# Optimization experiments

Measured on AMD Instinct MI355X. Metric: run time of the kernel, lower is better.

## Reference

```python
import jax, jax.numpy as jnp
import numpy as np

B, S, T = 1024, 1024, 32  # batch, seq_len, num_tags


def setup_inputs() -> dict:
    key = jax.random.key(0)
    k1, k2, k3, k4 = jax.random.split(key, 4)
    logits = jax.random.normal(k1, (B, S, T), dtype=jnp.float32)
    transitions = jax.random.normal(k2, (T, T), dtype=jnp.float32)
    tags = jax.random.randint(k3, (B, S), 0, T)
    lengths = jax.random.randint(k4, (B,), 1, S + 1)
    return {"logits": logits, "transitions": transitions, "tags": tags, "lengths": lengths}


def _forward_alg(logits, transitions):
    # viterbi_0 = logits[:, 0, :]; then for t>=1:
    # v_next[b, j] = logsumexp_i(v[b, i] + trans[i, j]) + logits[b, t, j]
    v0 = logits[:, 0, :]  # (B, T)
    emits = jnp.swapaxes(logits[:, 1:, :], 0, 1)  # (S-1, B, T)

    def step(v, emit_t):
        v_next = jax.nn.logsumexp(v[:, :, None] + transitions[None, :, :], axis=1) + emit_t
        return v_next, None

    v_final, _ = jax.lax.scan(step, v0, emits)
    return jax.nn.logsumexp(v_final, axis=1)  # (B,)


def _score_sentence(logits, transitions, tags, lengths):
    # emission scores of gold tags, masked to t < length (note: original ignores
    # lengths in the forward algorithm but uses them here, faithfully reproduced)
    emit = jnp.take_along_axis(logits, tags[:, :, None], axis=2)[..., 0]  # (B, S)
    pos = jnp.arange(S)
    emit_mask = (pos[None, :] < lengths[:, None]).astype(logits.dtype)
    score = jnp.sum(emit * emit_mask, axis=1)
    # transition scores trans[tags[t-1], tags[t]] for 1 <= t < length
    trans_sc = transitions[tags[:, :-1], tags[:, 1:]]  # (B, S-1)
    trans_mask = (pos[None, 1:] < lengths[:, None]).astype(logits.dtype)
    score = score + jnp.sum(trans_sc * trans_mask, axis=1)
    return score  # (B,)


def reference(logits, transitions, tags, lengths):
    log_z = _forward_alg(logits, transitions)
    gold = _score_sentence(logits, transitions, tags, lengths)
    return jnp.mean(log_z - gold)
```

## Files before the change

kernel.cpp:

```cpp
#include <hip/hip_runtime.h>

#define NB 1024
#define NS 1024
#define NT 32
#define L2E 1.44269504088896340736f
#define LN2 0.69314718055994530942f

typedef short        bfrag  __attribute__((ext_vector_type(8)));
typedef float        cfrag  __attribute__((ext_vector_type(16)));
typedef __bf16       bf16x2 __attribute__((ext_vector_type(2)));
typedef float        f32x8  __attribute__((ext_vector_type(8)));
typedef float        f32x4  __attribute__((ext_vector_type(4)));
typedef float        f32x2  __attribute__((ext_vector_type(2)));
typedef unsigned int u32;
typedef unsigned int u32x2v __attribute__((ext_vector_type(2)));
typedef unsigned int u32x4  __attribute__((ext_vector_type(4)));

__device__ __forceinline__ float fexp2(float x){ return __builtin_amdgcn_exp2f(x); }
__device__ __forceinline__ float flog2(float x){ return __builtin_amdgcn_logf(x); }

__device__ __forceinline__ u32 pkbf_rne(float a, float b){
    f32x2 t; t.x = a; t.y = b;
    return __builtin_bit_cast(u32, __builtin_convertvector(t, bf16x2));
}
__device__ __forceinline__ u32 pkbf_t(float a, float b){
    return __builtin_amdgcn_perm(__builtin_bit_cast(u32, b),
                                 __builtin_bit_cast(u32, a), 0x07060302u);
}
__device__ __forceinline__ bfrag mk_afrag(f32x8 v){
    u32x4 r;
    r[0] = pkbf_rne(v[0], v[1]); r[1] = pkbf_rne(v[2], v[3]);
    r[2] = pkbf_rne(v[4], v[5]); r[3] = pkbf_rne(v[6], v[7]);
    return __builtin_bit_cast(bfrag, r);
}

#if __has_builtin(__builtin_amdgcn_permlane32_swap)
#define HAVE_PLSWAP 1
#else
#define HAVE_PLSWAP 0
#endif

__device__ __forceinline__ void half_swap(u32 &x, u32 &y, int h){
#if HAVE_PLSWAP
    u32x2v r = __builtin_amdgcn_permlane32_swap(x, y, false, false);
    x = r[0]; y = r[1];
#else
    u32 X  = __shfl_xor(h ? x : y, 32, 64);
    u32 nx = h ? X : x;
    u32 ny = h ? y : X;
    x = nx; y = ny;
#endif
}

template<int N> struct ic { static constexpr int value = N; };
union accu { cfrag c; f32x2 p[8]; };
union q4u  { f32x4 v; f32x2 p[2]; };

__global__ __launch_bounds__(256, 8) void crf_chunk(
    const float* __restrict__ logits, const float* __restrict__ trans,
    u32* __restrict__ wmat, float* __restrict__ woff)
{
    __shared__ __align__(16) float dscall[4 * 512];

    const int tid = threadIdx.x;
    const int wv  = tid >> 6, lt = tid & 63;
    const int m   = lt & 31,  h  = lt >> 5;
    const int bc  = blockIdx.x * 4 + wv;
    const int b   = bc >> 3,  c  = bc & 7;
    float* dsc = dscall + wv * 512;

    const float* base = logits + (size_t)b * NS * NT;

    f32x8 Et0, Et1;
    #pragma unroll
    for (int j = 0; j < 8; j++){
        Et0[j] = fexp2(L2E * trans[(     8*h + j)*NT + m]);
        Et1[j] = fexp2(L2E * trans[(16 + 8*h + j)*NT + m]);
    }
    const bfrag A0f = mk_afrag(Et0);
    const bfrag A1f = mk_afrag(Et1);

    u32x4 B0v, B1v;
    #pragma unroll
    for (int d = 0; d < 4; d++){
        int k0 = 8*h + 2*d;      u32 v = 0;
        if (k0     == m) v |= 0x3F80u;
        if (k0 + 1 == m) v |= 0x3F800000u;
        B0v[d] = v;
        int k1 = 16 + 8*h + 2*d; v = 0;
        if (k1     == m) v |= 0x3F80u;
        if (k1 + 1 == m) v |= 0x3F800000u;
        B1v[d] = v;
    }

    cfrag zacc;
    #pragma unroll
    for (int q = 0; q < 16; q++) zacc[q] = 0.0f;

    int   offi = 0;
    float exf  = 0.0f;
    const int tbeg = c*128 + 1;

    float eA[4], eB[4];

    auto issue = [&](float (&e)[4], int k){
        const int t0 = tbeg + k*8 + 4*h;
        #pragma unroll
        for (int i = 0; i < 4; i++){
            int t = t0 + i; t = t > (NS-1) ? (NS-1) : t;
            e[i] = base[t*NT + m];
        }
    };
    auto commit = [&](float (&e)[4], int k){
        float* sp = dsc + (k & 1)*256 + (4*h)*32 + m;
        float a0 = (h == 0) ? -exf : 0.0f;
        sp[0]    = fexp2(fmaf(L2E, e[0], a0));
        sp[32]   = fexp2(L2E * e[1]);
        sp[64]   = fexp2(L2E * e[2]);
        sp[96]   = fexp2(L2E * e[3]);
    };

    auto exref = [&](float ref)->int{
        u32 xb = __builtin_bit_cast(u32, ref);
        u32 xf = __builtin_amdgcn_readfirstlane(xb);
        int ex = (int)((xf >> 23) & 0xFFu) - 127;
        return ex < -120 ? -120 : (ex > 120 ? 120 : ex);
    };

    auto procN = [&](int k, bool defer, auto nstc){
        constexpr int NST = decltype(nstc)::value;
        const float* db = dsc + (k & 1)*256 + 4*h;
        #pragma unroll
        for (int i = 0; i < NST; i++){
            accu acc;
            acc.c = __builtin_amdgcn_mfma_f32_32x32x16_bf16(
                        A0f, __builtin_bit_cast(bfrag, B0v), zacc, 0, 0, 0);
            acc.c = __builtin_amdgcn_mfma_f32_32x32x16_bf16(
                        A1f, __builtin_bit_cast(bfrag, B1v), acc.c, 0, 0, 0);

            q4u d0, d1, d2, d3;
            d0.v = *(const f32x4*)(db + i*32 +  0);
            d1.v = *(const f32x4*)(db + i*32 +  8);
            d2.v = *(const f32x4*)(db + i*32 + 16);
            d3.v = *(const f32x4*)(db + i*32 + 24);
            acc.p[0] *= d0.p[0]; acc.p[1] *= d0.p[1];
            acc.p[2] *= d1.p[0]; acc.p[3] *= d1.p[1];
            acc.p[4] *= d2.p[0]; acc.p[5] *= d2.p[1];
            acc.p[6] *= d3.p[0]; acc.p[7] *= d3.p[1];

            if (i == 3){
                int ex = exref(fmaxf(acc.c[0], acc.c[8]));
                offi += ex;
                f32x2 s2;
                s2.x = s2.y = __builtin_bit_cast(float, (u32)(127 - ex) << 23);
                #pragma unroll
                for (int q = 0; q < 8; q++) acc.p[q] *= s2;
            }
            if (i == 7 && defer){
                int ex = exref(fmaxf(acc.c[0], acc.c[8]));
                offi += ex;
                exf = (float)ex;
            }

            u32 P0 = pkbf_t(acc.c[0],  acc.c[1]),  P1 = pkbf_t(acc.c[2],  acc.c[3]);
            u32 P2 = pkbf_t(acc.c[4],  acc.c[5]),  P3 = pkbf_t(acc.c[6],  acc.c[7]);
            u32 P4 = pkbf_t(acc.c[8],  acc.c[9]),  P5 = pkbf_t(acc.c[10], acc.c[11]);
            u32 P6 = pkbf_t(acc.c[12], acc.c[13]), P7 = pkbf_t(acc.c[14], acc.c[15]);
            half_swap(P0, P2, h); half_swap(P1, P3, h);
            half_swap(P4, P6, h); half_swap(P5, P7, h);
            B0v[0]=P0; B0v[1]=P1; B0v[2]=P2; B0v[3]=P3;
            B1v[0]=P4; B1v[1]=P5; B1v[2]=P6; B1v[3]=P7;
        }
    };

    issue(eA, 0); commit(eA, 0);
    #pragma unroll 1
    for (int k = 0; k < 14; k += 2){
        issue(eB, k + 1);
        procN(k, true, ic<8>{});
        commit(eB, k + 1);
        issue(eA, k + 2);
        procN(k + 1, true, ic<8>{});
        commit(eA, k + 2);
    }
    issue(eB, 15);
    procN(14, true, ic<8>{});
    commit(eB, 15);
    if (c != 7) procN(15, false, ic<8>{});
    else        procN(15, false, ic<7>{});

    const size_t mb = (size_t)bc * 512;
    #pragma unroll
    for (int d = 0; d < 4; d++){
        wmat[mb + d*64 + lt]     = B0v[d];
        wmat[mb + (4+d)*64 + lt] = B1v[d];
    }
    if (lt == 0) woff[bc] = (float)offi;
}

__global__ __launch_bounds__(64) void crf_combine(
    const float* __restrict__ logits, const float* __restrict__ trans,
    const int* __restrict__ tags, const int* __restrict__ lens,
    const u32* __restrict__ wmat, const float* __restrict__ woff,
    float* __restrict__ out)
{
    __shared__ __align__(16) float ldsT[NT*NT];
    __shared__ __align__(16) int   ldsTag[NS];
    __shared__ __align__(16) float ldsU[NT];

    const int tid = threadIdx.x;
    const int m   = tid & 31;
    const int b   = blockIdx.x;
    const int len = lens[b];
    const float* lgb = logits + (size_t)b * NS * NT;

    #pragma unroll
    for (int i = 0; i < 16; i++) ldsT[tid + i*64] = trans[tid + i*64];
    const int4* tg4 = (const int4*)(tags + b*NS);
    #pragma unroll
    for (int i = 0; i < 4; i++) ((int4*)ldsTag)[tid + i*64] = tg4[tid + i*64];
    __syncthreads();

    float g = 0.0f;
    #pragma unroll
    for (int it = 0; it < 16; it++){
        int t = tid + it*64;
        if (t < len){
            int tg = ldsTag[t];
            g += lgb[t*NT + tg];
            if (t >= 1) g += ldsT[ldsTag[t-1]*NT + tg];
        }
    }

    float v = fexp2(L2E * lgb[m]);
    float voff = 0.0f;

    const int n  = m;
    const int f  = n >> 4;
    const int hh = (n >> 3) & 1;
    const int di = f*4 + ((n >> 1) & 3);

    for (int cc = 0; cc < 8; cc++){
        const int bcn = b*8 + cc;
        float offc = woff[bcn];
        float w = flog2(v) + offc;
        float mw = w;
        #pragma unroll
        for (int d = 1; d <= 16; d <<= 1) mw = fmaxf(mw, __shfl_xor(mw, d, 64));
        float u = fexp2(w - mw);
        if (tid < 32) ldsU[m] = u;
        __syncthreads();

        const uint4* mp = (const uint4*)(wmat + (size_t)bcn*512 + di*64 + hh*32);
        float acc = 0.0f;
        #pragma unroll
        for (int qq = 0; qq < 8; qq++){
            uint4  md = mp[qq];
            float4 uu = ((const float4*)ldsU)[qq];
            float e0 = __builtin_bit_cast(float, (n&1) ? (md.x & 0xFFFF0000u) : (md.x << 16));
            float e1 = __builtin_bit_cast(float, (n&1) ? (md.y & 0xFFFF0000u) : (md.y << 16));
            float e2 = __builtin_bit_cast(float, (n&1) ? (md.z & 0xFFFF0000u) : (md.z << 16));
            float e3 = __builtin_bit_cast(float, (n&1) ? (md.w & 0xFFFF0000u) : (md.w << 16));
            acc = fmaf(e0, uu.x, acc);
            acc = fmaf(e1, uu.y, acc);
            acc = fmaf(e2, uu.z, acc);
            acc = fmaf(e3, uu.w, acc);
        }
        v = acc;
        voff += mw;
        __syncthreads();
    }

    float s = v;
    #pragma unroll
    for (int d = 1; d <= 16; d <<= 1) s += __shfl_xor(s, d, 64);
    #pragma unroll
    for (int d = 1; d <= 32; d <<= 1) g += __shfl_xor(g, d, 64);
    if (tid == 0){
        float logz = LN2 * (voff + flog2(s));
        atomicAdd(out, (logz - g) * (1.0f / (float)NB));
    }
}

extern "C" void kernel_launch(void* const* d_in, const int* in_sizes, int n_in,
                              void* d_out, int out_size, void* d_ws, size_t ws_size,
                              hipStream_t stream) {
    const float* logits = (const float*)d_in[0];
    const float* trans  = (const float*)d_in[1];
    const int*   tags   = (const int*)d_in[2];
    const int*   lens   = (const int*)d_in[3];

    u32*   wmat = (u32*)d_ws;
    float* woff = (float*)(wmat + 8192*512);

    hipMemsetAsync(d_out, 0, sizeof(float), stream);
    crf_chunk  <<<2048, 256, 0, stream>>>(logits, trans, wmat, woff);
    crf_combine<<<1024, 64, 0, stream>>>(logits, trans, tags, lens, wmat, woff,
                                         (float*)d_out);
}
```

Before: 263.7 us.

## Fold emission scaling into MFMA A-operand and drop LDS staging

Instead of multiplying the MFMA output by per-row emission factors staged through shared memory, each step rebuilds the A fragment as exp(trans) scaled by exp(emission) and packs it to bf16. The per-block rescale multiply on the accumulator is also folded into the next step's emission factor. This removes the LDS writes and reads and the post-MFMA multiplies, and loads each thread's emissions directly into registers with triple buffering. In exchange it adds eight packed multiplies and bf16 packs per step, uses more registers (launch bounds lowered from 8 to 4 blocks per CU), and truncates the scaled matrix to bf16 rather than rounding it.

```diff
diff --git a/kernel.cpp b/kernel.cpp
--- a/kernel.cpp
+++ b/kernel.cpp
@@ -9,8 +9,6 @@
 typedef short        bfrag  __attribute__((ext_vector_type(8)));
 typedef float        cfrag  __attribute__((ext_vector_type(16)));
 typedef __bf16       bf16x2 __attribute__((ext_vector_type(2)));
-typedef float        f32x8  __attribute__((ext_vector_type(8)));
-typedef float        f32x4  __attribute__((ext_vector_type(4)));
 typedef float        f32x2  __attribute__((ext_vector_type(2)));
 typedef unsigned int u32;
 typedef unsigned int u32x2v __attribute__((ext_vector_type(2)));
@@ -19,19 +17,9 @@
 __device__ __forceinline__ float fexp2(float x){ return __builtin_amdgcn_exp2f(x); }
 __device__ __forceinline__ float flog2(float x){ return __builtin_amdgcn_logf(x); }
 
-__device__ __forceinline__ u32 pkbf_rne(float a, float b){
-    f32x2 t; t.x = a; t.y = b;
-    return __builtin_bit_cast(u32, __builtin_convertvector(t, bf16x2));
-}
 __device__ __forceinline__ u32 pkbf_t(float a, float b){
     return __builtin_amdgcn_perm(__builtin_bit_cast(u32, b),
                                  __builtin_bit_cast(u32, a), 0x07060302u);
-}
-__device__ __forceinline__ bfrag mk_afrag(f32x8 v){
-    u32x4 r;
-    r[0] = pkbf_rne(v[0], v[1]); r[1] = pkbf_rne(v[2], v[3]);
-    r[2] = pkbf_rne(v[4], v[5]); r[3] = pkbf_rne(v[6], v[7]);
-    return __builtin_bit_cast(bfrag, r);
 }
 
 #if __has_builtin(__builtin_amdgcn_permlane32_swap)
@@ -54,31 +42,30 @@
 
 template<int N> struct ic { static constexpr int value = N; };
 union accu { cfrag c; f32x2 p[8]; };
-union q4u  { f32x4 v; f32x2 p[2]; };
-
-__global__ __launch_bounds__(256, 8) void crf_chunk(
+
+__global__ __launch_bounds__(256, 4) void crf_chunk(
     const float* __restrict__ logits, const float* __restrict__ trans,
     u32* __restrict__ wmat, float* __restrict__ woff)
 {
-    __shared__ __align__(16) float dscall[4 * 512];
-
     const int tid = threadIdx.x;
     const int wv  = tid >> 6, lt = tid & 63;
     const int m   = lt & 31,  h  = lt >> 5;
     const int bc  = blockIdx.x * 4 + wv;
     const int b   = bc >> 3,  c  = bc & 7;
-    float* dsc = dscall + wv * 512;
-
-    const float* base = logits + (size_t)b * NS * NT;
-
-    f32x8 Et0, Et1;
-    #pragma unroll
-    for (int j = 0; j < 8; j++){
-        Et0[j] = fexp2(L2E * trans[(     8*h + j)*NT + m]);
-        Et1[j] = fexp2(L2E * trans[(16 + 8*h + j)*NT + m]);
-    }
-    const bfrag A0f = mk_afrag(Et0);
-    const bfrag A1f = mk_afrag(Et1);
+
+    const int tbeg = c*128 + 1;
+    const int L    = (c == 7) ? 127 : 128;
+    const int Lm1  = L - 1;
+    const float* p = logits + (size_t)b * NS * NT + (size_t)tbeg * NT + m;
+
+    f32x2 Et0p[4], Et1p[4];
+    #pragma unroll
+    for (int d = 0; d < 4; d++){
+        Et0p[d].x = fexp2(L2E * trans[(     8*h + 2*d    )*NT + m]);
+        Et0p[d].y = fexp2(L2E * trans[(     8*h + 2*d + 1)*NT + m]);
+        Et1p[d].x = fexp2(L2E * trans[(16 + 8*h + 2*d    )*NT + m]);
+        Et1p[d].y = fexp2(L2E * trans[(16 + 8*h + 2*d + 1)*NT + m]);
+    }
 
     u32x4 B0v, B1v;
     #pragma unroll
@@ -98,68 +85,45 @@
     for (int q = 0; q < 16; q++) zacc[q] = 0.0f;
 
     int   offi = 0;
-    float exf  = 0.0f;
-    const int tbeg = c*128 + 1;
-
-    float eA[4], eB[4];
-
-    auto issue = [&](float (&e)[4], int k){
-        const int t0 = tbeg + k*8 + 4*h;
-        #pragma unroll
-        for (int i = 0; i < 4; i++){
-            int t = t0 + i; t = t > (NS-1) ? (NS-1) : t;
-            e[i] = base[t*NT + m];
+    float adj  = 0.0f;
+
+    float e0[8], e1[8], e2[8];
+    auto loadblk = [&](float (&e)[8], int k){
+        #pragma unroll
+        for (int i = 0; i < 8; i++){
+            int t = k*8 + i; t = t > Lm1 ? Lm1 : t;
+            e[i] = p[t*NT];
         }
     };
-    auto commit = [&](float (&e)[4], int k){
-        float* sp = dsc + (k & 1)*256 + (4*h)*32 + m;
-        float a0 = (h == 0) ? -exf : 0.0f;
-        sp[0]    = fexp2(fmaf(L2E, e[0], a0));
-        sp[32]   = fexp2(L2E * e[1]);
-        sp[64]   = fexp2(L2E * e[2]);
-        sp[96]   = fexp2(L2E * e[3]);
-    };
-
-    auto exref = [&](float ref)->int{
-        u32 xb = __builtin_bit_cast(u32, ref);
-        u32 xf = __builtin_amdgcn_readfirstlane(xb);
-        int ex = (int)((xf >> 23) & 0xFFu) - 127;
-        return ex < -120 ? -120 : (ex > 120 ? 120 : ex);
-    };
-
-    auto procN = [&](int k, bool defer, auto nstc){
+
+    auto procblk = [&](float (&e)[8], bool last, auto nstc){
         constexpr int NST = decltype(nstc)::value;
-        const float* db = dsc + (k & 1)*256 + 4*h;
         #pragma unroll
         for (int i = 0; i < NST; i++){
+            float dval = (i == 0 || i == 4) ? fexp2(fmaf(L2E, e[i], adj))
+                                            : fexp2(L2E * e[i]);
+            f32x2 ds; ds.x = dval; ds.y = dval;
+            u32x4 a0, a1;
+            #pragma unroll
+            for (int d = 0; d < 4; d++){
+                f32x2 t0 = Et0p[d] * ds;  a0[d] = pkbf_t(t0.x, t0.y);
+                f32x2 t1 = Et1p[d] * ds;  a1[d] = pkbf_t(t1.x, t1.y);
+            }
             accu acc;
             acc.c = __builtin_amdgcn_mfma_f32_32x32x16_bf16(
-                        A0f, __builtin_bit_cast(bfrag, B0v), zacc, 0, 0, 0);
+                        __builtin_bit_cast(bfrag, a0),
+                        __builtin_bit_cast(bfrag, B0v), zacc, 0, 0, 0);
             acc.c = __builtin_amdgcn_mfma_f32_32x32x16_bf16(
-                        A1f, __builtin_bit_cast(bfrag, B1v), acc.c, 0, 0, 0);
-
-            q4u d0, d1, d2, d3;
-            d0.v = *(const f32x4*)(db + i*32 +  0);
-            d1.v = *(const f32x4*)(db + i*32 +  8);
-            d2.v = *(const f32x4*)(db + i*32 + 16);
-            d3.v = *(const f32x4*)(db + i*32 + 24);
-            acc.p[0] *= d0.p[0]; acc.p[1] *= d0.p[1];
-            acc.p[2] *= d1.p[0]; acc.p[3] *= d1.p[1];
-            acc.p[4] *= d2.p[0]; acc.p[5] *= d2.p[1];
-            acc.p[6] *= d3.p[0]; acc.p[7] *= d3.p[1];
-
-            if (i == 3){
-                int ex = exref(fmaxf(acc.c[0], acc.c[8]));
+                        __builtin_bit_cast(bfrag, a1),
+                        __builtin_bit_cast(bfrag, B1v), acc.c, 0, 0, 0);
+
+            if (i == 3 || (i == 7 && !last)){
+                float ref = fmaxf(acc.c[0], acc.c[8]);
+                u32 xf = __builtin_amdgcn_readfirstlane(__builtin_bit_cast(u32, ref));
+                int ex = (int)((xf >> 23) & 0xFFu) - 127;
+                ex = ex < -120 ? -120 : (ex > 120 ? 120 : ex);
                 offi += ex;
-                f32x2 s2;
-                s2.x = s2.y = __builtin_bit_cast(float, (u32)(127 - ex) << 23);
-                #pragma unroll
-                for (int q = 0; q < 8; q++) acc.p[q] *= s2;
-            }
-            if (i == 7 && defer){
-                int ex = exref(fmaxf(acc.c[0], acc.c[8]));
-                offi += ex;
-                exf = (float)ex;
+                adj = -(float)ex;
             }
 
             u32 P0 = pkbf_t(acc.c[0],  acc.c[1]),  P1 = pkbf_t(acc.c[2],  acc.c[3]);
@@ -173,21 +137,18 @@
         }
     };
 
-    issue(eA, 0); commit(eA, 0);
+    loadblk(e0, 0); loadblk(e1, 1);
     #pragma unroll 1
-    for (int k = 0; k < 14; k += 2){
-        issue(eB, k + 1);
-        procN(k, true, ic<8>{});
-        commit(eB, k + 1);
-        issue(eA, k + 2);
-        procN(k + 1, true, ic<8>{});
-        commit(eA, k + 2);
-    }
-    issue(eB, 15);
-    procN(14, true, ic<8>{});
-    commit(eB, 15);
-    if (c != 7) procN(15, false, ic<8>{});
-    else        procN(15, false, ic<7>{});
+    for (int k = 0; k < 15; k += 3){
+        loadblk(e2, k + 2);
+        procblk(e0, false, ic<8>{});
+        if (k + 3 < 16) loadblk(e0, k + 3);
+        procblk(e1, false, ic<8>{});
+        if (k + 4 < 16) loadblk(e1, k + 4);
+        procblk(e2, false, ic<8>{});
+    }
+    if (c != 7) procblk(e0, true, ic<8>{});
+    else        procblk(e0, true, ic<7>{});
 
     const size_t mb = (size_t)bc * 512;
     #pragma unroll
```

After: 275.7 us. 4.6% more time.
